# Performance work log

Measured on AMD Instinct MI355X. Metric: run time of the kernel, lower is better.

The kernel has to match this reference:

```python
import jax, jax.numpy as jnp
import numpy as np

NUM_GROUPS = 32
EPS = 1e-6


def setup_inputs() -> dict:
    key = jax.random.key(0)
    ks = jax.random.split(key, 11)
    b, c, h, w = 4, 512, 64, 64
    s = 0.02
    return {
        "x": jax.random.normal(ks[0], (b, c, h, w), dtype=jnp.float32),
        "gn_w": jnp.ones((c,), dtype=jnp.float32),
        "gn_b": jnp.zeros((c,), dtype=jnp.float32),
        "wq": jax.random.normal(ks[1], (c, c), dtype=jnp.float32) * s,
        "bq": jax.random.normal(ks[2], (c,), dtype=jnp.float32) * s,
        "wk": jax.random.normal(ks[3], (c, c), dtype=jnp.float32) * s,
        "bk": jax.random.normal(ks[4], (c,), dtype=jnp.float32) * s,
        "wv": jax.random.normal(ks[5], (c, c), dtype=jnp.float32) * s,
        "bv": jax.random.normal(ks[6], (c,), dtype=jnp.float32) * s,
        "wo": jax.random.normal(ks[7], (c, c), dtype=jnp.float32) * s,
        "bo": jax.random.normal(ks[8], (c,), dtype=jnp.float32) * s,
    }


def _group_norm(x, gamma, beta):
    b, c, h, w = x.shape
    g = NUM_GROUPS
    xg = x.reshape(b, g, c // g, h, w)
    mean = jnp.mean(xg, axis=(2, 3, 4), keepdims=True)
    var = jnp.var(xg, axis=(2, 3, 4), keepdims=True)
    xg = (xg - mean) * jax.lax.rsqrt(var + EPS)
    x = xg.reshape(b, c, h, w)
    return x * gamma[None, :, None, None] + beta[None, :, None, None]


def _conv1x1(x, wmat, bias):
    # x: [b,c,h,w], wmat: [out,in] -> [b,out,h,w]
    return jnp.einsum('bchw,oc->bohw', x, wmat) + bias[None, :, None, None]


def reference(x, gn_w, gn_b, wq, bq, wk, bk, wv, bv, wo, bo):
    b, c, h, w = x.shape
    h_ = _group_norm(x, gn_w, gn_b)
    q = _conv1x1(h_, wq, bq).reshape(b, c, h * w)  # [b,c,hw]
    k = _conv1x1(h_, wk, bk).reshape(b, c, h * w)
    v = _conv1x1(h_, wv, bv).reshape(b, c, h * w)
    scale = float(c) ** (-0.5)
    # scores[b,i,j] = sum_c q[b,c,i] * k[b,c,j]
    scores = jnp.einsum('bci,bcj->bij', q, k) * scale
    attn = jax.nn.softmax(scores, axis=2)  # softmax over j (keys)
    # out[b,c,i] = sum_j v[b,c,j] * attn[b,i,j]
    out = jnp.einsum('bcj,bij->bci', v, attn).reshape(b, c, h, w)
    out = _conv1x1(out, wo, bo)
    return x + out
```

## Files before the change

### kernel.cpp

```cpp
#include <hip/hip_runtime.h>
#include <math.h>

using short8 = __attribute__((ext_vector_type(8))) short;
using f32x4  = __attribute__((ext_vector_type(4))) float;
using i32x8  = __attribute__((ext_vector_type(8))) int;

__device__ __forceinline__ ushort f2bf(float f) {
    union { float f; uint u; } c; c.f = f;
    uint u = c.u;
    uint r = (u + 0x7FFFu + ((u >> 16) & 1u)) >> 16;
    return (ushort)r;
}
__device__ __forceinline__ unsigned char f2fp8(float x) {
    return (unsigned char)__builtin_amdgcn_cvt_pk_fp8_f32(x, 0.f, 0, false);
}

__device__ __forceinline__ void gload16(const void* g, void* l) {
    __builtin_amdgcn_global_load_lds(
        (const __attribute__((address_space(1))) unsigned int*)g,
        (__attribute__((address_space(3))) unsigned int*)l,
        16, 0, 0);
}

__global__ __launch_bounds__(256) void prep_weights(
    const float* __restrict__ wq, const float* __restrict__ bq,
    const float* __restrict__ wk, const float* __restrict__ bk,
    const float* __restrict__ wv, const float* __restrict__ wo,
    ushort* __restrict__ Wqk, ushort* __restrict__ Wv, ushort* __restrict__ Wo,
    float* __restrict__ bqk, float* __restrict__ stats, float scale)
{
    int idx = blockIdx.x * 256 + threadIdx.x;
    if (idx < 1024 * 512) {
        float v = (idx < 262144) ? wq[idx] * scale : wk[idx - 262144];
        Wqk[idx] = f2bf(v);
    }
    if (idx < 262144) {
        Wv[idx] = f2bf(wv[idx]);
        Wo[idx] = f2bf(wo[idx]);
    }
    if (idx < 1024) bqk[idx] = (idx < 512) ? bq[idx] * scale : bk[idx - 512];
    if (idx < 256) stats[idx] = 0.f;
}

__global__ __launch_bounds__(256) void gn_stats(
    const float* __restrict__ x, float* __restrict__ stats)
{
    int blk = blockIdx.x;
    int grp = blk >> 3, sub = blk & 7;
    const float* xp = x + (size_t)grp * 65536 + sub * 8192;
    int tid = threadIdx.x;

    float s = 0.f, sq = 0.f;
    #pragma unroll
    for (int j = 0; j < 8; ++j) {
        float4 v = *(const float4*)&xp[tid * 4 + j * 1024];
        s  += v.x + v.y + v.z + v.w;
        sq += v.x * v.x + v.y * v.y + v.z * v.z + v.w * v.w;
    }
    #pragma unroll
    for (int off = 32; off; off >>= 1) {
        s  += __shfl_xor(s,  off, 64);
        sq += __shfl_xor(sq, off, 64);
    }
    __shared__ float red[8];
    if ((tid & 63) == 0) { red[(tid >> 6) * 2] = s; red[(tid >> 6) * 2 + 1] = sq; }
    __syncthreads();
    if (tid == 0) {
        atomicAdd(&stats[grp * 2],     red[0] + red[2] + red[4] + red[6]);
        atomicAdd(&stats[grp * 2 + 1], red[1] + red[3] + red[5] + red[7]);
    }
}

__global__ __launch_bounds__(256) void gn_apply(
    const float* __restrict__ x, const float* __restrict__ gamma,
    const float* __restrict__ beta, const float* __restrict__ stats,
    ushort* __restrict__ hnt)
{
    int blk = blockIdx.x;
    int grp = blk >> 4, tile = blk & 15;
    int b = grp >> 5, g = grp & 31;
    const float* xp = x + (size_t)grp * 65536;
    int tid = threadIdx.x;

    float mean = stats[grp * 2] * (1.f / 65536.f);
    float var  = stats[grp * 2 + 1] * (1.f / 65536.f) - mean * mean;
    float rstd = rsqrtf(var + 1e-6f);

    int i0 = tile * 256;
    __shared__ ushort ls[16][256];
    #pragma unroll
    for (int ch = 0; ch < 16; ++ch) {
        float a = rstd * gamma[g * 16 + ch];
        float c = beta[g * 16 + ch] - mean * a;
        ls[ch][tid] = f2bf(xp[ch * 4096 + i0 + tid] * a + c);
    }
    __syncthreads();
    ushort t[16];
    #pragma unroll
    for (int ch = 0; ch < 16; ++ch) t[ch] = ls[ch][tid];
    size_t dst = ((size_t)b * 4096 + i0 + tid) * 512 + g * 16;
    *(uint4*)&hnt[dst]     = *(const uint4*)&t[0];
    *(uint4*)&hnt[dst + 8] = *(const uint4*)&t[8];
}

template <int BIAS, int OUT>
__global__ __launch_bounds__(256, 4) void gemm_nt(
    const ushort* __restrict__ Ag, const ushort* __restrict__ Bg,
    void* __restrict__ Cv, void* __restrict__ Cv2,
    const float* __restrict__ bias, const float* __restrict__ resid,
    int N, int K, int lda, int ldb,
    long sA, long sB, long sC)
{
    const int bz = blockIdx.z;
    Ag += (size_t)bz * sA;
    Bg += (size_t)bz * sB;

    const int tid  = threadIdx.x;
    const int wave = tid >> 6, lane = tid & 63;
    const int q = lane >> 4, lr = lane & 15;
    const int m0 = blockIdx.x * 128, n0 = blockIdx.y * 128;
    const int wm = (wave >> 1) * 64, wn = (wave & 1) * 64;

    __shared__ __align__(16) ushort As[2][128 * 32];
    __shared__ __align__(16) ushort Bs[2][128 * 32];

    const int srow = wave * 32 + (lane >> 2);
    const int skc  = (lane & 3) << 3;
    const size_t aoff0 = (size_t)(m0 + srow) * lda + skc;
    const size_t aoff1 = aoff0 + (size_t)16 * lda;
    const size_t boff0 = (size_t)(n0 + srow) * ldb + skc;
    const size_t boff1 = boff0 + (size_t)16 * ldb;
    const int l0 = wave * 1024, l1 = wave * 1024 + 512;

    f32x4 acc[4][4] = {};

    for (int kb = 0; kb < K; kb += 64) {
        __syncthreads();
        gload16(&Ag[aoff0 + kb],      &As[0][l0]);
        gload16(&Ag[aoff1 + kb],      &As[0][l1]);
        gload16(&Ag[aoff0 + kb + 32], &As[1][l0]);
        gload16(&Ag[aoff1 + kb + 32], &As[1][l1]);
        gload16(&Bg[boff0 + kb],      &Bs[0][l0]);
        gload16(&Bg[boff1 + kb],      &Bs[0][l1]);
        gload16(&Bg[boff0 + kb + 32], &Bs[1][l0]);
        gload16(&Bg[boff1 + kb + 32], &Bs[1][l1]);
        __syncthreads();

        #pragma unroll
        for (int kh = 0; kh < 2; ++kh) {
            short8 af[4], bfr[4];
            #pragma unroll
            for (int mt = 0; mt < 4; ++mt)
                af[mt] = *(const short8*)&As[kh][(wm + mt * 16 + lr) * 32 + q * 8];
            #pragma unroll
            for (int nt = 0; nt < 4; ++nt)
                bfr[nt] = *(const short8*)&Bs[kh][(wn + nt * 16 + lr) * 32 + q * 8];
            #pragma unroll
            for (int mt = 0; mt < 4; ++mt)
                #pragma unroll
                for (int nt = 0; nt < 4; ++nt)
                    acc[mt][nt] = __builtin_amdgcn_mfma_f32_16x16x32_bf16(
                        af[mt], bfr[nt], acc[mt][nt], 0, 0, 0);
        }
    }

    if (OUT == 2 || OUT == 3) {
        __syncthreads();
        unsigned char* C8 = (unsigned char*)&As[0][0];
        #pragma unroll
        for (int mt = 0; mt < 4; ++mt) {
            #pragma unroll
            for (int nt = 0; nt < 4; ++nt) {
                int col = wn + nt * 16 + lr;
                #pragma unroll
                for (int t = 0; t < 4; ++t) {
                    int row = wm + mt * 16 + q * 4 + t;
                    float v = acc[mt][nt][t];
                    if (BIAS == 1) v += bias[m0 + row];
                    if (BIAS == 2) v += bias[n0 + col];
                    if (OUT == 3 && n0 < 512) v *= 16.f;
                    C8[row * 128 + ((((col >> 4) ^ (row & 7)) << 4) | (col & 15))]
                        = f2fp8(v);
                }
            }
        }
        __syncthreads();
        const int er = tid >> 3, eck = tid & 7;
        #pragma unroll
        for (int p = 0; p < 4; ++p) {
            int row = p * 32 + er;
            uint4 v = *(const uint4*)&C8[row * 128 + ((eck ^ (row & 7)) << 4)];
            if (OUT == 2) {
                *(uint4*)&((unsigned char*)Cv)[(size_t)bz * sC
                    + (size_t)(m0 + row) * N + n0 + eck * 16] = v;
            } else {
                if (n0 < 512)
                    *(uint4*)&((unsigned char*)Cv)[(size_t)bz * sC
                        + (size_t)(m0 + row) * 512 + n0 + eck * 16] = v;
                else
                    *(uint4*)&((unsigned char*)Cv2)[(size_t)bz * sC
                        + (size_t)(m0 + row) * 512 + (n0 - 512) + eck * 16] = v;
            }
        }
        return;
    }

    #pragma unroll
    for (int mt = 0; mt < 4; ++mt) {
        int rb = m0 + wm + mt * 16 + q * 4;
        #pragma unroll
        for (int nt = 0; nt < 4; ++nt) {
            int cn = n0 + wn + nt * 16 + lr;
            #pragma unroll
            for (int t = 0; t < 4; ++t) {
                int r = rb + t;
                float v = acc[mt][nt][t];
                if (BIAS == 1) v += bias[r];
                if (BIAS == 2) v += bias[cn];
                if (OUT == 1) {
                    size_t o = (size_t)bz * sC + (size_t)r * N + cn;
                    ((float*)Cv)[o] = v + resid[o];
                } else {
                    size_t o = (size_t)bz * sC + (size_t)r * N + cn;
                    ((ushort*)Cv)[o] = f2bf(v);
                }
            }
        }
    }
}

__global__ __launch_bounds__(256, 2) void gemm_qk(
    const unsigned char* __restrict__ Q8, const unsigned char* __restrict__ K8,
    unsigned char* __restrict__ P8, float* __restrict__ Zpart)
{
    const int bz = blockIdx.z;
    const unsigned char* Ag = Q8 + (size_t)bz * 2097152;
    const unsigned char* Bg = K8 + (size_t)bz * 2097152;

    const int tid  = threadIdx.x;
    const int wave = tid >> 6, lane = tid & 63;
    const int q = lane >> 4, lr = lane & 15;
    const int m0 = blockIdx.x * 128, n0 = blockIdx.y * 128;
    const int wm = (wave >> 1) * 64, wn = (wave & 1) * 64;

    __shared__ __align__(16) unsigned char smem[32768];
    __shared__ float Zs[2][128];
    unsigned char* As = smem;
    unsigned char* Bs = smem + 16384;
    unsigned char* C8 = smem;

    const int lrow = lane >> 3;
    const size_t laneoff = (size_t)lrow * 512 + ((lane & 7) ^ (lrow & 7)) * 16;
    const size_t abase = (size_t)(m0 + wave * 32) * 512 + laneoff;
    const size_t bbase = (size_t)(n0 + wave * 32) * 512 + laneoff;
    unsigned char* lA = As + wave * 32 * 128;
    unsigned char* lB = Bs + wave * 32 * 128;

    const int e0 = (2 * q) ^ (lr & 7), e1 = e0 ^ 1;

    f32x4 acc[4][4] = {};
    const int sA = 0x7B7B7B7B;
    const int sB = 0x7F7F7F7F;

    for (int kb = 0; kb < 512; kb += 128) {
        __syncthreads();
        #pragma unroll
        for (int t = 0; t < 4; ++t) {
            gload16(Ag + abase + (size_t)t * 4096 + kb, lA + t * 1024);
            gload16(Bg + bbase + (size_t)t * 4096 + kb, lB + t * 1024);
        }
        __syncthreads();

        i32x8 af[4], bf[4];
        #pragma unroll
        for (int mt = 0; mt < 4; ++mt) {
            int r = wm + mt * 16 + lr;
            union { uint4 v[2]; i32x8 f; } u;
            u.v[0] = *(const uint4*)&As[r * 128 + e0 * 16];
            u.v[1] = *(const uint4*)&As[r * 128 + e1 * 16];
            af[mt] = u.f;
        }
        #pragma unroll
        for (int nt = 0; nt < 4; ++nt) {
            int r = wn + nt * 16 + lr;
            union { uint4 v[2]; i32x8 f; } u;
            u.v[0] = *(const uint4*)&Bs[r * 128 + e0 * 16];
            u.v[1] = *(const uint4*)&Bs[r * 128 + e1 * 16];
            bf[nt] = u.f;
        }
        #pragma unroll
        for (int mt = 0; mt < 4; ++mt)
            #pragma unroll
            for (int nt = 0; nt < 4; ++nt)
                acc[mt][nt] = __builtin_amdgcn_mfma_scale_f32_16x16x128_f8f6f4(
                    af[mt], bf[nt], acc[mt][nt], 0, 0, 0, sA, 0, sB);
    }

    #pragma unroll
    for (int mt = 0; mt < 4; ++mt)
        #pragma unroll
        for (int nt = 0; nt < 4; ++nt)
            #pragma unroll
            for (int t = 0; t < 4; ++t)
                acc[mt][nt][t] = __expf(acc[mt][nt][t]) * 32.f;

    __syncthreads();
    #pragma unroll
    for (int mt = 0; mt < 4; ++mt) {
        #pragma unroll
        for (int nt = 0; nt < 4; ++nt) {
            int col = wn + nt * 16 + lr;
            #pragma unroll
            for (int t = 0; t < 4; ++t) {
                int row = wm + mt * 16 + q * 4 + t;
                C8[row * 128 + ((((col >> 4) ^ (row & 7)) << 4) | (col & 15))]
                    = f2fp8(acc[mt][nt][t]);
            }
        }
    }

    #pragma unroll
    for (int mt = 0; mt < 4; ++mt) {
        #pragma unroll
        for (int t = 0; t < 4; ++t) {
            float rs = acc[mt][0][t] + acc[mt][1][t]
                     + acc[mt][2][t] + acc[mt][3][t];
            #pragma unroll
            for (int off = 1; off < 16; off <<= 1)
                rs += __shfl_xor(rs, off, 64);
            if (lr == 0)
                Zs[wave & 1][wm + mt * 16 + q * 4 + t] = rs;
        }
    }

    __syncthreads();
    if (tid < 128)
        Zpart[(size_t)bz * 131072 + (size_t)blockIdx.y * 4096 + m0 + tid]
            = Zs[0][tid] + Zs[1][tid];
    const int er = tid >> 3, eck = tid & 7;
    unsigned char* orow = P8 + (size_t)bz * 16777216 + (size_t)m0 * 4096 + n0;
    #pragma unroll
    for (int p = 0; p < 4; ++p) {
        int row = p * 32 + er;
        uint4 v = *(const uint4*)&C8[row * 128 + ((eck ^ (row & 7)) << 4)];
        *(uint4*)&orow[(size_t)row * 4096 + eck * 16] = v;
    }
}

__global__ __launch_bounds__(256, 2) void gemm_pv(
    const unsigned char* __restrict__ P8, const unsigned char* __restrict__ V8,
    ushort* __restrict__ Ot, const float* __restrict__ Zpart)
{
    const int bz = blockIdx.z;
    const unsigned char* Ag = P8 + (size_t)bz * 16777216;
    const unsigned char* Bg = V8 + (size_t)bz * 2097152;

    const int tid  = threadIdx.x;
    const int wave = tid >> 6, lane = tid & 63;
    const int q = lane >> 4, lr = lane & 15;
    const int m0 = blockIdx.x * 128, n0 = blockIdx.y * 128;
    const int wm = (wave >> 1) * 64, wn = (wave & 1) * 64;

    __shared__ __align__(16) unsigned char smem[32768];
    __shared__ float Zr[128];
    unsigned char* As = smem;
    unsigned char* Bs = smem + 16384;
    ushort* Cs = (ushort*)smem;

    if (tid < 128) {
        const float* zp = Zpart + (size_t)bz * 131072 + m0 + tid;
        float z = 0.f;
        #pragma unroll
        for (int by = 0; by < 32; ++by) z += zp[by * 4096];
        Zr[tid] = 1.0f / z;
    }

    const int lrow = lane >> 3;
    const size_t laneoff = (size_t)lrow * 4096 + ((lane & 7) ^ (lrow & 7)) * 16;
    const size_t abase = (size_t)(m0 + wave * 32) * 4096 + laneoff;
    const size_t bbase = (size_t)(n0 + wave * 32) * 4096 + laneoff;
    unsigned char* lA = As + wave * 32 * 128;
    unsigned char* lB = Bs + wave * 32 * 128;

    const int e0 = (2 * q) ^ (lr & 7), e1 = e0 ^ 1;

    f32x4 acc[4][4] = {};
    const int sA = 0x7F7F7F7F;
    const int sB = 0x7F7F7F7F;

    for (int kb = 0; kb < 4096; kb += 128) {
        __syncthreads();
        #pragma unroll
        for (int t = 0; t < 4; ++t) {
            gload16(Ag + abase + (size_t)t * 32768 + kb, lA + t * 1024);
            gload16(Bg + bbase + (size_t)t * 32768 + kb, lB + t * 1024);
        }
        __syncthreads();

        i32x8 af[4], bf[4];
        #pragma unroll
        for (int mt = 0; mt < 4; ++mt) {
            int r = wm + mt * 16 + lr;
            union { uint4 v[2]; i32x8 f; } u;
            u.v[0] = *(const uint4*)&As[r * 128 + e0 * 16];
            u.v[1] = *(const uint4*)&As[r * 128 + e1 * 16];
            af[mt] = u.f;
        }
        #pragma unroll
        for (int nt = 0; nt < 4; ++nt) {
            int r = wn + nt * 16 + lr;
            union { uint4 v[2]; i32x8 f; } u;
            u.v[0] = *(const uint4*)&Bs[r * 128 + e0 * 16];
            u.v[1] = *(const uint4*)&Bs[r * 128 + e1 * 16];
            bf[nt] = u.f;
        }
        #pragma unroll
        for (int mt = 0; mt < 4; ++mt)
            #pragma unroll
            for (int nt = 0; nt < 4; ++nt)
                acc[mt][nt] = __builtin_amdgcn_mfma_scale_f32_16x16x128_f8f6f4(
                    af[mt], bf[nt], acc[mt][nt], 0, 0, 0, sA, 0, sB);
    }

    __syncthreads();
    #pragma unroll
    for (int mt = 0; mt < 4; ++mt) {
        #pragma unroll
        for (int t = 0; t < 4; ++t) {
            int row = wm + mt * 16 + q * 4 + t;
            float iz = Zr[row];
            #pragma unroll
            for (int nt = 0; nt < 4; ++nt) {
                int col = wn + nt * 16 + lr;
                Cs[row * 128 + ((((col >> 3) ^ (row & 7)) << 3) | (col & 7))]
                    = f2bf(acc[mt][nt][t] * iz);
            }
        }
    }
    __syncthreads();
    const int er = tid >> 4, eck = tid & 15;
    ushort* orow = Ot + (size_t)bz * 2097152 + (size_t)m0 * 512 + n0;
    #pragma unroll
    for (int p = 0; p < 8; ++p) {
        int row = p * 16 + er;
        uint4 v = *(const uint4*)&Cs[row * 128 + ((eck ^ (row & 7)) << 3)];
        *(uint4*)&orow[(size_t)row * 512 + eck * 8] = v;
    }
}

extern "C" void kernel_launch(void* const* d_in, const int* in_sizes, int n_in,
                              void* d_out, int out_size, void* d_ws, size_t ws_size,
                              hipStream_t stream)
{
    const float* x   = (const float*)d_in[0];
    const float* gnw = (const float*)d_in[1];
    const float* gnb = (const float*)d_in[2];
    const float* wq  = (const float*)d_in[3];
    const float* bq  = (const float*)d_in[4];
    const float* wk  = (const float*)d_in[5];
    const float* bk  = (const float*)d_in[6];
    const float* wv  = (const float*)d_in[7];
    const float* bv  = (const float*)d_in[8];
    const float* wo  = (const float*)d_in[9];
    const float* bo  = (const float*)d_in[10];
    float* out = (float*)d_out;

    char* ws = (char*)d_ws;
    unsigned char* P8  = (unsigned char*)(ws);
    ushort*        Ot  = (ushort*)(ws + 67108864);
    ushort*        hnt = (ushort*)(ws + 83886080);
    unsigned char* Q8  = (unsigned char*)(ws + 100663296);
    unsigned char* K8  = (unsigned char*)(ws + 109051904);
    unsigned char* V8  = (unsigned char*)(ws + 117440512);
    float*         Zp  = (float*) (ws + 125829120);
    ushort*        Wqk = (ushort*)(ws + 127926272);
    ushort*        Wv  = (ushort*)(ws + 128974848);
    ushort*        Wo  = (ushort*)(ws + 129499136);
    float*         bqk = (float*) (ws + 130023424);
    float*         st  = (float*) (ws + 130027520);

    const float scale = 1.0f / sqrtf(512.0f);
    const long sHW  = 512L * 4096;

    prep_weights<<<2048, 256, 0, stream>>>(wq, bq, wk, bk, wv, wo,
                                           Wqk, Wv, Wo, bqk, st, scale);
    gn_stats<<<1024, 256, 0, stream>>>(x, st);
    gn_apply<<<2048, 256, 0, stream>>>(x, gnw, gnb, st, hnt);

    gemm_nt<2, 3><<<dim3(32, 8, 4), 256, 0, stream>>>(
        hnt, Wqk, Q8, K8, bqk, nullptr,
        1024, 512, 512, 512, sHW, 0L, sHW);

    gemm_nt<1, 2><<<dim3(4, 32, 4), 256, 0, stream>>>(
        Wv, hnt, V8, nullptr, bv, nullptr,
        4096, 512, 512, 512, 0L, sHW, sHW);

    gemm_qk<<<dim3(32, 32, 4), 256, 0, stream>>>(Q8, K8, P8, Zp);

    gemm_pv<<<dim3(32, 4, 4), 256, 0, stream>>>(P8, V8, Ot, Zp);

    gemm_nt<1, 1><<<dim3(4, 32, 4), 256, 0, stream>>>(
        Wo, Ot, out, nullptr, bo, x,
        4096, 512, 512, 512, 0L, sHW, sHW);
}
```

Before: 271.6 us.

## Store packed FP8 epilogues directly from registers and drop LDS staging

The QK-exp epilogue and the V-projection epilogue now pack four FP8 values per lane and store them straight to global memory, skipping the LDS transpose and its barriers. This permutes columns within each 64-wide chunk, so P and V8 must share the same key ordering for the PV product to stay correct. The row-sum shuffle reduction is replaced by per-lane partials written to LDS and summed by 128 threads. gemm_qk's launch bound is raised to 4 blocks per CU to allow more occupancy. The trade-off is narrower 4-byte scattered stores in place of 16-byte coalesced ones, and tighter register limits that may cause spills.

```diff
diff --git a/kernel.cpp b/kernel.cpp
--- a/kernel.cpp
+++ b/kernel.cpp
@@ -13,6 +13,11 @@
 }
 __device__ __forceinline__ unsigned char f2fp8(float x) {
     return (unsigned char)__builtin_amdgcn_cvt_pk_fp8_f32(x, 0.f, 0, false);
+}
+__device__ __forceinline__ uint pk4_fp8(float a, float b, float c, float d) {
+    int v = __builtin_amdgcn_cvt_pk_fp8_f32(a, b, 0, false);
+    v = __builtin_amdgcn_cvt_pk_fp8_f32(c, d, v, true);
+    return (uint)v;
 }
 
 __device__ __forceinline__ void gload16(const void* g, void* l) {
@@ -164,7 +169,23 @@
         }
     }
 
-    if (OUT == 2 || OUT == 3) {
+    if (OUT == 2) {
+        #pragma unroll
+        for (int mt = 0; mt < 4; ++mt) {
+            #pragma unroll
+            for (int t = 0; t < 4; ++t) {
+                int row = m0 + wm + mt * 16 + q * 4 + t;
+                float b = (BIAS == 1) ? bias[row] : 0.f;
+                uint d = pk4_fp8(acc[mt][0][t] + b, acc[mt][1][t] + b,
+                                 acc[mt][2][t] + b, acc[mt][3][t] + b);
+                *(uint*)&((unsigned char*)Cv)[(size_t)bz * sC
+                    + (size_t)row * N + n0 + wn + lr * 4] = d;
+            }
+        }
+        return;
+    }
+
+    if (OUT == 3) {
         __syncthreads();
         unsigned char* C8 = (unsigned char*)&As[0][0];
         #pragma unroll
@@ -178,7 +199,7 @@
                     float v = acc[mt][nt][t];
                     if (BIAS == 1) v += bias[m0 + row];
                     if (BIAS == 2) v += bias[n0 + col];
-                    if (OUT == 3 && n0 < 512) v *= 16.f;
+                    if (n0 < 512) v *= 16.f;
                     C8[row * 128 + ((((col >> 4) ^ (row & 7)) << 4) | (col & 15))]
                         = f2fp8(v);
                 }
@@ -190,17 +211,12 @@
         for (int p = 0; p < 4; ++p) {
             int row = p * 32 + er;
             uint4 v = *(const uint4*)&C8[row * 128 + ((eck ^ (row & 7)) << 4)];
-            if (OUT == 2) {
+            if (n0 < 512)
                 *(uint4*)&((unsigned char*)Cv)[(size_t)bz * sC
-                    + (size_t)(m0 + row) * N + n0 + eck * 16] = v;
-            } else {
-                if (n0 < 512)
-                    *(uint4*)&((unsigned char*)Cv)[(size_t)bz * sC
-                        + (size_t)(m0 + row) * 512 + n0 + eck * 16] = v;
-                else
-                    *(uint4*)&((unsigned char*)Cv2)[(size_t)bz * sC
-                        + (size_t)(m0 + row) * 512 + (n0 - 512) + eck * 16] = v;
-            }
+                    + (size_t)(m0 + row) * 512 + n0 + eck * 16] = v;
+            else
+                *(uint4*)&((unsigned char*)Cv2)[(size_t)bz * sC
+                    + (size_t)(m0 + row) * 512 + (n0 - 512) + eck * 16] = v;
         }
         return;
     }
@@ -229,7 +245,7 @@
     }
 }
 
-__global__ __launch_bounds__(256, 2) void gemm_qk(
+__global__ __launch_bounds__(256, 4) void gemm_qk(
     const unsigned char* __restrict__ Q8, const unsigned char* __restrict__ K8,
     unsigned char* __restrict__ P8, float* __restrict__ Zpart)
 {
@@ -244,10 +260,9 @@
     const int wm = (wave >> 1) * 64, wn = (wave & 1) * 64;
 
     __shared__ __align__(16) unsigned char smem[32768];
-    __shared__ float Zs[2][128];
     unsigned char* As = smem;
     unsigned char* Bs = smem + 16384;
-    unsigned char* C8 = smem;
+    float* Zs = (float*)Bs;
 
     const int lrow = lane >> 3;
     const size_t laneoff = (size_t)lrow * 512 + ((lane & 7) ^ (lrow & 7)) * 16;
@@ -296,54 +311,41 @@
                     af[mt], bf[nt], acc[mt][nt], 0, 0, 0, sA, 0, sB);
     }
 
+    float rs[4][4];
+    unsigned char* prow = P8 + (size_t)bz * 16777216 + (size_t)m0 * 4096
+                        + n0 + wn + lr * 4;
+    #pragma unroll
+    for (int mt = 0; mt < 4; ++mt) {
+        #pragma unroll
+        for (int t = 0; t < 4; ++t) {
+            float e0v = __expf(acc[mt][0][t]) * 32.f;
+            float e1v = __expf(acc[mt][1][t]) * 32.f;
+            float e2v = __expf(acc[mt][2][t]) * 32.f;
+            float e3v = __expf(acc[mt][3][t]) * 32.f;
+            rs[mt][t] = (e0v + e1v) + (e2v + e3v);
+            uint d = pk4_fp8(e0v, e1v, e2v, e3v);
+            *(uint*)&prow[(size_t)(wm + mt * 16 + q * 4 + t) * 4096] = d;
+        }
+    }
+
+    __syncthreads();
     #pragma unroll
     for (int mt = 0; mt < 4; ++mt)
         #pragma unroll
-        for (int nt = 0; nt < 4; ++nt)
-            #pragma unroll
-            for (int t = 0; t < 4; ++t)
-                acc[mt][nt][t] = __expf(acc[mt][nt][t]) * 32.f;
-
+        for (int t = 0; t < 4; ++t)
+            Zs[((wave & 1) * 128 + wm + mt * 16 + q * 4 + t) * 16 + lr]
+                = rs[mt][t];
     __syncthreads();
-    #pragma unroll
-    for (int mt = 0; mt < 4; ++mt) {
-        #pragma unroll
-        for (int nt = 0; nt < 4; ++nt) {
-            int col = wn + nt * 16 + lr;
-            #pragma unroll
-            for (int t = 0; t < 4; ++t) {
-                int row = wm + mt * 16 + q * 4 + t;
-                C8[row * 128 + ((((col >> 4) ^ (row & 7)) << 4) | (col & 15))]
-                    = f2fp8(acc[mt][nt][t]);
-            }
-        }
-    }
-
-    #pragma unroll
-    for (int mt = 0; mt < 4; ++mt) {
-        #pragma unroll
-        for (int t = 0; t < 4; ++t) {
-            float rs = acc[mt][0][t] + acc[mt][1][t]
-                     + acc[mt][2][t] + acc[mt][3][t];
-            #pragma unroll
-            for (int off = 1; off < 16; off <<= 1)
-                rs += __shfl_xor(rs, off, 64);
-            if (lr == 0)
-                Zs[wave & 1][wm + mt * 16 + q * 4 + t] = rs;
-        }
-    }
-
-    __syncthreads();
-    if (tid < 128)
-        Zpart[(size_t)bz * 131072 + (size_t)blockIdx.y * 4096 + m0 + tid]
-            = Zs[0][tid] + Zs[1][tid];
-    const int er = tid >> 3, eck = tid & 7;
-    unsigned char* orow = P8 + (size_t)bz * 16777216 + (size_t)m0 * 4096 + n0;
-    #pragma unroll
-    for (int p = 0; p < 4; ++p) {
-        int row = p * 32 + er;
-        uint4 v = *(const uint4*)&C8[row * 128 + ((eck ^ (row & 7)) << 4)];
-        *(uint4*)&orow[(size_t)row * 4096 + eck * 16] = v;
+    if (tid < 128) {
+        const float4* z0 = (const float4*)&Zs[tid * 16];
+        const float4* z1 = (const float4*)&Zs[2048 + tid * 16];
+        float4 a0 = z0[0], a1 = z0[1], a2 = z0[2], a3 = z0[3];
+        float4 b0 = z1[0], b1 = z1[1], b2 = z1[2], b3 = z1[3];
+        float z = ((a0.x + a0.y + a0.z + a0.w) + (a1.x + a1.y + a1.z + a1.w))
+                + ((a2.x + a2.y + a2.z + a2.w) + (a3.x + a3.y + a3.z + a3.w))
+                + ((b0.x + b0.y + b0.z + b0.w) + (b1.x + b1.y + b1.z + b1.w))
+                + ((b2.x + b2.y + b2.z + b2.w) + (b3.x + b3.y + b3.z + b3.w));
+        Zpart[(size_t)bz * 131072 + (size_t)blockIdx.y * 4096 + m0 + tid] = z;
     }
 }
 
```

Result: no change. 269.5 us (-0.8%).
